# Kernel optimization log

Measured on AMD Instinct MI355X. Metric: run time of the kernel, lower is better.

The kernel has to match this reference:

```python
import jax, jax.numpy as jnp
import numpy as np

U, I, K = 50000, 30000, 64
D0, D1 = 768, 128
N_INTER = 1_000_000
N_LAYERS = 3
BATCH = 4096
EPS = 1e-12


def setup_inputs() -> dict:
    key = jax.random.key(0)
    k1, k2, k3, k4 = jax.random.split(key, 4)
    rng = np.random.default_rng(0)
    # bidirectional bipartite edges: user u <-> item node (U + i)
    u = rng.integers(0, U, size=N_INTER)
    i = rng.integers(0, I, size=N_INTER) + U
    src = np.concatenate([u, i])
    dst = np.concatenate([i, u])
    edge_index = jnp.asarray(np.stack([src, dst]), dtype=jnp.int32)  # [2, 2*N_INTER]
    return {
        "Gu": jax.random.normal(k1, (U, K), dtype=jnp.float32) * 0.1,
        "F0": jax.random.normal(k2, (I, D0), dtype=jnp.float32),
        "F1": jax.random.normal(k3, (I, D1), dtype=jnp.float32),
        "proj_w": jax.random.normal(k4, (D0 + D1, K), dtype=jnp.float32) * 0.03,
        "proj_b": jnp.zeros((K,), dtype=jnp.float32),
        "edge_index": edge_index,
        "user_idx": jnp.asarray(rng.integers(0, U, size=BATCH), dtype=jnp.int32),
        "item_idx": jnp.asarray(rng.integers(0, I, size=BATCH), dtype=jnp.int32),
    }


def _l2_normalize(x):
    # torch.nn.functional.normalize(p=2, dim=1) with eps clamp
    n = jnp.maximum(jnp.linalg.norm(x, axis=1, keepdims=True), EPS)
    return x / n


def reference(Gu, F0, F1, proj_w, proj_b, edge_index, user_idx, item_idx):
    N = U + I
    # concat aggregation: project concatenated multimodal features, L2-normalize rows
    F_proj = _l2_normalize(jnp.concatenate([F0, F1], axis=-1) @ proj_w + proj_b)
    x = jnp.concatenate([Gu, F_proj], axis=0)  # [N, K]

    src, dst = edge_index[0], edge_index[1]
    # gcn_norm without self-loops (LGConv default): D^{-1/2} A D^{-1/2}
    deg = jax.ops.segment_sum(jnp.ones(src.shape[0], dtype=x.dtype), dst, num_segments=N)
    dinv = jnp.where(deg > 0, jax.lax.rsqrt(jnp.maximum(deg, 1.0)), 0.0)
    norm = dinv[src] * dinv[dst]  # [E]

    layers = [x]
    for _ in range(N_LAYERS):
        msg = layers[-1][src] * norm[:, None]  # [E, K]
        layers.append(jax.ops.segment_sum(msg, dst, num_segments=N))

    all_emb = jnp.mean(jnp.stack(layers, axis=0), axis=0)  # layer-wise mean pooling
    gu, fi = all_emb[:U], all_emb[U:]

    # forward(): batched dot product between selected user/item embeddings
    xui = jnp.sum(gu[user_idx] * fi[item_idx], axis=1)  # [BATCH]
    return xui
```

## Files before the change

kernel.cpp:

```cpp
#include <hip/hip_runtime.h>
#include <hip/hip_bf16.h>

#define NU 50000
#define NI 30000
#define NN 80000
#define KDIM 64
#define DD0 768
#define DD1 128
#define DD 896

#define BROWS 128
#define NB (NN / BROWS)
#define CAPB 5120
#define CAP 96
#define REGION_BYTES 24576
#define ENTS_STRIDE (REGION_BYTES / 4)
#define CHUNK_PAIRS 4096

typedef __attribute__((ext_vector_type(8))) short short8v;
typedef __attribute__((ext_vector_type(4))) short short4v;
typedef __attribute__((ext_vector_type(4))) float float4v;
typedef unsigned short ushort_t;

struct bf16pair { short hi, lo; };

__device__ inline bf16pair f32_split_bf16(float v) {
    __hip_bfloat16 h = __float2bfloat16(v);
    float hf = __bfloat162float(h);
    __hip_bfloat16 l = __float2bfloat16(v - hf);
    bf16pair p;
    p.hi = *reinterpret_cast<short*>(&h);
    p.lo = *reinterpret_cast<short*>(&l);
    return p;
}

__device__ inline float bf16bits_to_f32(ushort_t u) {
    return __uint_as_float(((unsigned int)u) << 16);
}

__device__ inline ushort_t f32_to_bf16_rne(float f) {
    unsigned int u = __float_as_uint(f);
    unsigned int r = (u + 0x7FFFu + ((u >> 16) & 1u)) >> 16;
    return (ushort_t)r;
}

__global__ void wtcvt_kernel(const float* __restrict__ W,
                             short* __restrict__ WTh, short* __restrict__ WTl)
{
    const int i = blockIdx.x * 256 + threadIdx.x;
    if (i < DD * KDIM) {
        const int k = i >> 6, col = i & 63;
        const bf16pair p = f32_split_bf16(W[i]);
        WTh[col * DD + k] = p.hi;
        WTl[col * DD + k] = p.lo;
    }
}

__global__ __launch_bounds__(256) void proj_kernel(
    const float* __restrict__ F0, const float* __restrict__ F1,
    const short* __restrict__ WTh, const short* __restrict__ WTl,
    const float* __restrict__ b, const float* __restrict__ dinv,
    float* __restrict__ Fp, ushort_t* __restrict__ curS)
{
    __shared__ short Ah[64][72];
    __shared__ short Al[64][72];
    __shared__ short Bh[64][72];
    __shared__ short Bl[64][72];

    const int tid  = threadIdx.x;
    const int wv   = tid >> 6;
    const int lane = tid & 63;
    const int lr   = lane & 15;
    const int grp  = lane >> 4;
    const int rowBase = blockIdx.x * 64;

    const int aR[4] = { (0*256+tid) >> 4, (1*256+tid) >> 4,
                        (2*256+tid) >> 4, (3*256+tid) >> 4 };
    const int aK    = (tid & 15) * 4;
    const int bCol[2] = { (0*256+tid) >> 3, (1*256+tid) >> 3 };
    const int bK      = (tid & 7) * 8;

    float4   pA[4];
    short8v  pBh[2], pBl[2];

    auto loadChunk = [&](int c) {
        #pragma unroll
        for (int rep = 0; rep < 4; ++rep) {
            const int r = rowBase + aR[rep];
            float4 v = make_float4(0.f, 0.f, 0.f, 0.f);
            if (r < NI) {
                if (c < 12)
                    v = *(const float4*)&F0[(size_t)r * DD0 + c * 64 + aK];
                else
                    v = *(const float4*)&F1[(size_t)r * DD1 + (c - 12) * 64 + aK];
            }
            pA[rep] = v;
        }
        #pragma unroll
        for (int rep = 0; rep < 2; ++rep) {
            pBh[rep] = *(const short8v*)&WTh[(size_t)bCol[rep] * DD + c * 64 + bK];
            pBl[rep] = *(const short8v*)&WTl[(size_t)bCol[rep] * DD + c * 64 + bK];
        }
    };

    float4v acc[4] = {};

    loadChunk(0);
    for (int c = 0; c < 14; ++c) {
        #pragma unroll
        for (int rep = 0; rep < 4; ++rep) {
            const float4 v = pA[rep];
            const bf16pair p0 = f32_split_bf16(v.x);
            const bf16pair p1 = f32_split_bf16(v.y);
            const bf16pair p2 = f32_split_bf16(v.z);
            const bf16pair p3 = f32_split_bf16(v.w);
            short4v h4, l4;
            h4[0] = p0.hi; h4[1] = p1.hi; h4[2] = p2.hi; h4[3] = p3.hi;
            l4[0] = p0.lo; l4[1] = p1.lo; l4[2] = p2.lo; l4[3] = p3.lo;
            *(short4v*)&Ah[aR[rep]][aK] = h4;
            *(short4v*)&Al[aR[rep]][aK] = l4;
        }
        #pragma unroll
        for (int rep = 0; rep < 2; ++rep) {
            *(short8v*)&Bh[bCol[rep]][bK] = pBh[rep];
            *(short8v*)&Bl[bCol[rep]][bK] = pBl[rep];
        }
        if (c < 13) loadChunk(c + 1);
        __syncthreads();

        #pragma unroll
        for (int ks = 0; ks < 2; ++ks) {
            const int ko = ks * 32 + grp * 8;
            const short8v ah = *(const short8v*)&Ah[wv * 16 + lr][ko];
            const short8v al = *(const short8v*)&Al[wv * 16 + lr][ko];
            #pragma unroll
            for (int nt = 0; nt < 4; ++nt) {
                const short8v bh = *(const short8v*)&Bh[nt * 16 + lr][ko];
                const short8v bl = *(const short8v*)&Bl[nt * 16 + lr][ko];
                acc[nt] = __builtin_amdgcn_mfma_f32_16x16x32_bf16(ah, bh, acc[nt], 0, 0, 0);
                acc[nt] = __builtin_amdgcn_mfma_f32_16x16x32_bf16(ah, bl, acc[nt], 0, 0, 0);
                acc[nt] = __builtin_amdgcn_mfma_f32_16x16x32_bf16(al, bh, acc[nt], 0, 0, 0);
            }
        }
        __syncthreads();
    }

    float bias[4];
    #pragma unroll
    for (int nt = 0; nt < 4; ++nt) bias[nt] = b[nt * 16 + lr];

    float y[4][4];
    float ssp[4];
    #pragma unroll
    for (int i = 0; i < 4; ++i) {
        ssp[i] = 0.f;
        #pragma unroll
        for (int nt = 0; nt < 4; ++nt) {
            y[nt][i] = acc[nt][i] + bias[nt];
            ssp[i] += y[nt][i] * y[nt][i];
        }
    }
    #pragma unroll
    for (int i = 0; i < 4; ++i) {
        float ss = ssp[i];
        ss += __shfl_xor(ss, 1);
        ss += __shfl_xor(ss, 2);
        ss += __shfl_xor(ss, 4);
        ss += __shfl_xor(ss, 8);
        const int r = rowBase + wv * 16 + 4 * grp + i;
        if (r < NI) {
            const float inv = 1.0f / fmaxf(sqrtf(ss), 1e-12f);
            const float dv  = dinv[NU + r];
            #pragma unroll
            for (int nt = 0; nt < 4; ++nt) {
                const float o = y[nt][i] * inv;
                Fp[(size_t)(NU + r) * KDIM + nt * 16 + lr] = o;
                curS[(size_t)(NU + r) * KDIM + nt * 16 + lr] = f32_to_bf16_rne(o * dv);
            }
        }
    }
}

__global__ void userinit_kernel(const float* __restrict__ Gu,
                                const float* __restrict__ dinv,
                                ushort_t* __restrict__ curS)
{
    const int i = blockIdx.x * blockDim.x + threadIdx.x;
    if (i < NU * KDIM / 4) {
        const int row = i >> 4;
        const float dv = dinv[row];
        const float4 g = ((const float4*)Gu)[i];
        short4v s;
        s[0] = (short)f32_to_bf16_rne(g.x * dv);
        s[1] = (short)f32_to_bf16_rne(g.y * dv);
        s[2] = (short)f32_to_bf16_rne(g.z * dv);
        s[3] = (short)f32_to_bf16_rne(g.w * dv);
        *(short4v*)&curS[(size_t)i * 4] = s;
    }
}

__global__ __launch_bounds__(256) void part_kernel(
    const int* __restrict__ src, const int* __restrict__ dst,
    int* __restrict__ bcur, unsigned int* __restrict__ ents, int E2)
{
    __shared__ int bcntL[NB];
    __shared__ int bposL[NB];
    const int tid = threadIdx.x;
    const int pairBase = blockIdx.x * CHUNK_PAIRS;

    for (int i = tid; i < NB; i += 256) bcntL[i] = 0;
    __syncthreads();

    #pragma unroll
    for (int it = 0; it < CHUNK_PAIRS / 256; ++it) {
        const int p = pairBase + it * 256 + tid;
        if (p < E2) {
            const int u  = src[p];
            const int iF = dst[p];
            atomicAdd(&bcntL[iF >> 7], 1);
            atomicAdd(&bcntL[u  >> 7], 1);
        }
    }
    __syncthreads();

    for (int bkt = tid; bkt < NB; bkt += 256) {
        const int c = bcntL[bkt];
        bposL[bkt] = (c > 0) ? atomicAdd(&bcur[bkt], c) : 0;
        bcntL[bkt] = 0;
    }
    __syncthreads();

    #pragma unroll
    for (int it = 0; it < CHUNK_PAIRS / 256; ++it) {
        const int p = pairBase + it * 256 + tid;
        if (p < E2) {
            const int u  = src[p];
            const int iF = dst[p];
            {
                const int bkt = iF >> 7;
                const int k = bposL[bkt] + atomicAdd(&bcntL[bkt], 1);
                if (k < CAPB)
                    ents[(size_t)bkt * ENTS_STRIDE + k] =
                        ((unsigned int)(iF & 127) << 16) | (unsigned int)u;
            }
            {
                const int bkt = u >> 7;
                const int k = bposL[bkt] + atomicAdd(&bcntL[bkt], 1);
                if (k < CAPB)
                    ents[(size_t)bkt * ENTS_STRIDE + k] =
                        ((unsigned int)(u & 127) << 16) | (unsigned int)(iF - NU);
            }
        }
    }
}

__global__ __launch_bounds__(256) void toELL_kernel(
    const int* __restrict__ bcur, unsigned int* __restrict__ ents,
    ushort_t* __restrict__ col,
    int* __restrict__ cnt, float* __restrict__ dinv)
{
    __shared__ unsigned int eL[CAPB];
    __shared__ int curL[BROWS];
    const int bkt = blockIdx.x;
    const int tid = threadIdx.x;

    int n = bcur[bkt]; n = (n < CAPB) ? n : CAPB;
    const unsigned int* ep = ents + (size_t)bkt * ENTS_STRIDE;

    for (int j = tid; j < n; j += 256) eL[j] = ep[j];
    if (tid < BROWS) curL[tid] = 0;
    __syncthreads();

    const size_t rowB = (size_t)bkt * BROWS;
    for (int j = tid; j < n; j += 256) {
        const unsigned int e = eL[j];
        const int dl = (int)(e >> 16);
        const int slot = atomicAdd(&curL[dl], 1);
        if (slot < CAP)
            col[(rowB + dl) * CAP + slot] = (ushort_t)(e & 0xFFFFu);
    }
    __syncthreads();

    if (tid < BROWS) {
        int c = curL[tid];
        c = (c < CAP) ? c : CAP;
        const size_t row = rowB + tid;
        cnt[row]  = c;
        dinv[row] = (c > 0) ? rsqrtf((float)c) : 0.0f;
    }
}

__global__ __launch_bounds__(256) void pull_kernel(
    const ushort_t* __restrict__ curS, ushort_t* __restrict__ nxtS,
    const int* __restrict__ cnt,
    const ushort_t* __restrict__ col,
    const float* __restrict__ dinv,
    int rowStart, int nRows)
{
    const int wid = __builtin_amdgcn_readfirstlane(
        (int)((blockIdx.x * blockDim.x + threadIdx.x) >> 6));
    const int lane = threadIdx.x & 63;
    if (wid >= nRows) return;
    const int row = rowStart + wid;

    const unsigned int* cpd = (const unsigned int*)(col + (size_t)row * CAP);
    const int addB = (row < NU) ? NU : 0;
    const int n = cnt[row];

    float a0 = 0.f, a1 = 0.f, a2 = 0.f, a3 = 0.f;
    int j = 0;
    for (; j + 8 <= n; j += 8) {
        const uint4 cc = *(const uint4*)(cpd + (j >> 1));
        const int c0 = (int)(cc.x & 0xFFFFu) + addB;
        const int c1 = (int)(cc.x >> 16)     + addB;
        const int c2 = (int)(cc.y & 0xFFFFu) + addB;
        const int c3 = (int)(cc.y >> 16)     + addB;
        const int c4 = (int)(cc.z & 0xFFFFu) + addB;
        const int c5 = (int)(cc.z >> 16)     + addB;
        const int c6 = (int)(cc.w & 0xFFFFu) + addB;
        const int c7 = (int)(cc.w >> 16)     + addB;
        const float v0 = bf16bits_to_f32(curS[((size_t)c0 << 6) + lane]);
        const float v1 = bf16bits_to_f32(curS[((size_t)c1 << 6) + lane]);
        const float v2 = bf16bits_to_f32(curS[((size_t)c2 << 6) + lane]);
        const float v3 = bf16bits_to_f32(curS[((size_t)c3 << 6) + lane]);
        const float v4 = bf16bits_to_f32(curS[((size_t)c4 << 6) + lane]);
        const float v5 = bf16bits_to_f32(curS[((size_t)c5 << 6) + lane]);
        const float v6 = bf16bits_to_f32(curS[((size_t)c6 << 6) + lane]);
        const float v7 = bf16bits_to_f32(curS[((size_t)c7 << 6) + lane]);
        a0 += v0 + v4; a1 += v1 + v5; a2 += v2 + v6; a3 += v3 + v7;
    }
    for (; j < n; ++j) {
        const unsigned int d = cpd[j >> 1];
        const int c = (int)((j & 1) ? (d >> 16) : (d & 0xFFFFu)) + addB;
        a0 += bf16bits_to_f32(curS[((size_t)c << 6) + lane]);
    }

    const float dv = dinv[row];
    nxtS[((size_t)row << 6) + lane] =
        f32_to_bf16_rne(dv * dv * ((a0 + a1) + (a2 + a3)));
}

__device__ inline float row_acc(int row, float x0, int lane,
                                const ushort_t* __restrict__ S1,
                                const ushort_t* __restrict__ S2,
                                const int* __restrict__ cnt,
                                const ushort_t* __restrict__ col,
                                const float* __restrict__ dinv)
{
    const float dv  = dinv[row];
    const float rdv = (dv > 0.f) ? 1.0f / dv : 0.0f;
    const float s1 = bf16bits_to_f32(S1[((size_t)row << 6) + lane]);
    const float s2 = bf16bits_to_f32(S2[((size_t)row << 6) + lane]);

    const unsigned int* cpd = (const unsigned int*)(col + (size_t)row * CAP);
    const int addB = (row < NU) ? NU : 0;
    const int n = cnt[row];
    float a0 = 0.f, a1 = 0.f, a2 = 0.f, a3 = 0.f;
    int j = 0;
    for (; j + 8 <= n; j += 8) {
        const uint4 cc = *(const uint4*)(cpd + (j >> 1));
        const int c0 = (int)(cc.x & 0xFFFFu) + addB;
        const int c1 = (int)(cc.x >> 16)     + addB;
        const int c2 = (int)(cc.y & 0xFFFFu) + addB;
        const int c3 = (int)(cc.y >> 16)     + addB;
        const int c4 = (int)(cc.z & 0xFFFFu) + addB;
        const int c5 = (int)(cc.z >> 16)     + addB;
        const int c6 = (int)(cc.w & 0xFFFFu) + addB;
        const int c7 = (int)(cc.w >> 16)     + addB;
        const float v0 = bf16bits_to_f32(S2[((size_t)c0 << 6) + lane]);
        const float v1 = bf16bits_to_f32(S2[((size_t)c1 << 6) + lane]);
        const float v2 = bf16bits_to_f32(S2[((size_t)c2 << 6) + lane]);
        const float v3 = bf16bits_to_f32(S2[((size_t)c3 << 6) + lane]);
        const float v4 = bf16bits_to_f32(S2[((size_t)c4 << 6) + lane]);
        const float v5 = bf16bits_to_f32(S2[((size_t)c5 << 6) + lane]);
        const float v6 = bf16bits_to_f32(S2[((size_t)c6 << 6) + lane]);
        const float v7 = bf16bits_to_f32(S2[((size_t)c7 << 6) + lane]);
        a0 += v0 + v4; a1 += v1 + v5; a2 += v2 + v6; a3 += v3 + v7;
    }
    for (; j < n; ++j) {
        const unsigned int d = cpd[j >> 1];
        const int c = (int)((j & 1) ? (d >> 16) : (d & 0xFFFFu)) + addB;
        a0 += bf16bits_to_f32(S2[((size_t)c << 6) + lane]);
    }

    return x0 + (s1 + s2) * rdv + dv * ((a0 + a1) + (a2 + a3));
}

__global__ __launch_bounds__(256) void out_kernel(
    const float* __restrict__ Gu, const float* __restrict__ Fp,
    const ushort_t* __restrict__ S1, const ushort_t* __restrict__ S2,
    const int* __restrict__ cnt, const ushort_t* __restrict__ col,
    const float* __restrict__ dinv,
    const int* __restrict__ uidx, const int* __restrict__ iidx,
    float* __restrict__ out, int B)
{
    const int wid = __builtin_amdgcn_readfirstlane(
        (int)((blockIdx.x * blockDim.x + threadIdx.x) >> 6));
    const int lane = threadIdx.x & 63;
    if (wid >= B) return;
    const int u  = uidx[wid];
    const int rI = NU + iidx[wid];

    const float au = row_acc(u,  Gu[((size_t)u  << 6) + lane], lane,
                             S1, S2, cnt, col, dinv);
    const float ai = row_acc(rI, Fp[((size_t)rI << 6) + lane], lane,
                             S1, S2, cnt, col, dinv);
    float p = au * ai;
    #pragma unroll
    for (int m = 32; m >= 1; m >>= 1) p += __shfl_xor(p, m);
    if (lane == 0) out[wid] = p * (1.0f / 16.0f);
}

extern "C" void kernel_launch(void* const* d_in, const int* in_sizes, int n_in,
                              void* d_out, int out_size, void* d_ws, size_t ws_size,
                              hipStream_t stream)
{
    const float* Gu = (const float*)d_in[0];
    const float* F0 = (const float*)d_in[1];
    const float* F1 = (const float*)d_in[2];
    const float* W  = (const float*)d_in[3];
    const float* pb = (const float*)d_in[4];
    const int* edge = (const int*)d_in[5];
    const int* uidx = (const int*)d_in[6];
    const int* iidx = (const int*)d_in[7];
    const int E  = in_sizes[5] / 2;
    const int E2 = E / 2;
    const int B = in_sizes[6];
    const int* srcp = edge;
    const int* dstp = edge + E;

    const size_t XE = (size_t)NN * KDIM;
    float*    Fp    = (float*)d_ws;
    ushort_t* curA  = (ushort_t*)(Fp + XE);
    ushort_t* curB  = curA + XE;
    float*    dinv  = (float*)(curB + XE);
    int*      cnt   = (int*)(dinv + NN);
    int*      bcur  = cnt + NN;
    short*    WTh   = (short*)(bcur + NB);
    short*    WTl   = WTh + (size_t)KDIM * DD;
    ushort_t* col   = (ushort_t*)(WTl + (size_t)KDIM * DD);
    unsigned int* ents = (unsigned int*)col;

    (void)hipMemsetAsync(bcur, 0, NB * sizeof(int), stream);
    part_kernel<<<(E2 + CHUNK_PAIRS - 1) / CHUNK_PAIRS, 256, 0, stream>>>(
        srcp, dstp, bcur, ents, E2);
    toELL_kernel<<<NB, 256, 0, stream>>>(bcur, ents, col, cnt, dinv);

    wtcvt_kernel<<<(DD * KDIM + 255) / 256, 256, 0, stream>>>(W, WTh, WTl);

    userinit_kernel<<<(NU * KDIM / 4 + 255) / 256, 256, 0, stream>>>(
        Gu, dinv, curA);
    proj_kernel<<<(NI + 63) / 64, 256, 0, stream>>>(F0, F1, WTh, WTl, pb,
                                                    dinv, Fp, curA);

    const int gridU = (NU * 64 + 255) / 256;
    const int gridI = (NI * 64 + 255) / 256;
    pull_kernel<<<gridU, 256, 0, stream>>>(curA, curB, cnt, col, dinv, 0, NU);
    pull_kernel<<<gridI, 256, 0, stream>>>(curA, curB, cnt, col, dinv, NU, NI);
    pull_kernel<<<gridU, 256, 0, stream>>>(curB, curA, cnt, col, dinv, 0, NU);
    pull_kernel<<<gridI, 256, 0, stream>>>(curB, curA, cnt, col, dinv, NU, NI);

    out_kernel<<<(int)(((size_t)B * 64 + 255) / 256), 256, 0, stream>>>(
        Gu, Fp, curB, curA, cnt, col, dinv, uidx, iidx, (float*)d_out, B);
}
```

Measured before the change: 178.3 us.

## Process two rows per wave in pull kernel and double-buffer projection prefetch

The graph pull kernel now assigns a pair of rows to each wave. Each half-wave gathers a full 64-wide bf16 row using 32-bit loads of packed element pairs, which halves the wave count and the number of gather instructions. The projection GEMM prefetches two chunks ahead with ping-pong register buffers to hide global latency better. The pull kernel risks divergence and a slow scalar tail when the two rows in a pair have different degrees, and the prefetch raises register pressure.

```diff
diff --git a/kernel.cpp b/kernel.cpp
--- a/kernel.cpp
+++ b/kernel.cpp
@@ -80,10 +80,11 @@
     const int bCol[2] = { (0*256+tid) >> 3, (1*256+tid) >> 3 };
     const int bK      = (tid & 7) * 8;
 
-    float4   pA[4];
-    short8v  pBh[2], pBl[2];
-
-    auto loadChunk = [&](int c) {
+    float4   pA0[4], pA1[4];
+    short8v  pBh0[2], pBl0[2], pBh1[2], pBl1[2];
+
+    auto loadChunk = [&](int c, float4 (&qA)[4],
+                         short8v (&qBh)[2], short8v (&qBl)[2]) {
         #pragma unroll
         for (int rep = 0; rep < 4; ++rep) {
             const int r = rowBase + aR[rep];
@@ -94,22 +95,22 @@
                 else
                     v = *(const float4*)&F1[(size_t)r * DD1 + (c - 12) * 64 + aK];
             }
-            pA[rep] = v;
+            qA[rep] = v;
         }
         #pragma unroll
         for (int rep = 0; rep < 2; ++rep) {
-            pBh[rep] = *(const short8v*)&WTh[(size_t)bCol[rep] * DD + c * 64 + bK];
-            pBl[rep] = *(const short8v*)&WTl[(size_t)bCol[rep] * DD + c * 64 + bK];
+            qBh[rep] = *(const short8v*)&WTh[(size_t)bCol[rep] * DD + c * 64 + bK];
+            qBl[rep] = *(const short8v*)&WTl[(size_t)bCol[rep] * DD + c * 64 + bK];
         }
     };
 
     float4v acc[4] = {};
 
-    loadChunk(0);
-    for (int c = 0; c < 14; ++c) {
+    auto step = [&](int c, float4 (&qA)[4],
+                    short8v (&qBh)[2], short8v (&qBl)[2]) {
         #pragma unroll
         for (int rep = 0; rep < 4; ++rep) {
-            const float4 v = pA[rep];
+            const float4 v = qA[rep];
             const bf16pair p0 = f32_split_bf16(v.x);
             const bf16pair p1 = f32_split_bf16(v.y);
             const bf16pair p2 = f32_split_bf16(v.z);
@@ -122,10 +123,10 @@
         }
         #pragma unroll
         for (int rep = 0; rep < 2; ++rep) {
-            *(short8v*)&Bh[bCol[rep]][bK] = pBh[rep];
-            *(short8v*)&Bl[bCol[rep]][bK] = pBl[rep];
-        }
-        if (c < 13) loadChunk(c + 1);
+            *(short8v*)&Bh[bCol[rep]][bK] = qBh[rep];
+            *(short8v*)&Bl[bCol[rep]][bK] = qBl[rep];
+        }
+        if (c + 2 < 14) loadChunk(c + 2, qA, qBh, qBl);
         __syncthreads();
 
         #pragma unroll
@@ -143,6 +144,14 @@
             }
         }
         __syncthreads();
+    };
+
+    loadChunk(0, pA0, pBh0, pBl0);
+    loadChunk(1, pA1, pBh1, pBl1);
+    #pragma unroll
+    for (int c = 0; c < 14; c += 2) {
+        step(c,     pA0, pBh0, pBl0);
+        step(c + 1, pA1, pBh1, pBl1);
     }
 
     float bias[4];
@@ -295,49 +304,82 @@
     const int* __restrict__ cnt,
     const ushort_t* __restrict__ col,
     const float* __restrict__ dinv,
-    int rowStart, int nRows)
-{
-    const int wid = __builtin_amdgcn_readfirstlane(
+    int rowStart, int nPairs)
+{
+    const int pr = __builtin_amdgcn_readfirstlane(
         (int)((blockIdx.x * blockDim.x + threadIdx.x) >> 6));
     const int lane = threadIdx.x & 63;
-    if (wid >= nRows) return;
-    const int row = rowStart + wid;
-
-    const unsigned int* cpd = (const unsigned int*)(col + (size_t)row * CAP);
-    const int addB = (row < NU) ? NU : 0;
-    const int n = cnt[row];
-
-    float a0 = 0.f, a1 = 0.f, a2 = 0.f, a3 = 0.f;
+    const int sub  = lane & 31;
+    const int h    = lane >> 5;
+    if (pr >= nPairs) return;
+    const int row0 = rowStart + pr * 2;
+    const int rowH = row0 + h;
+    const int addB = (row0 < NU) ? NU : 0;
+    const int n0 = cnt[row0];
+    const int n1 = cnt[row0 + 1];
+    const int nH   = h ? n1 : n0;
+    const int nMin = (n0 < n1) ? n0 : n1;
+    const int nMax = (n0 < n1) ? n1 : n0;
+    const unsigned int* cp0 = (const unsigned int*)(col + (size_t)row0 * CAP);
+    const unsigned int* cp1 = (const unsigned int*)(col + ((size_t)row0 + 1) * CAP);
+
+    float aLo0 = 0.f, aLo1 = 0.f, aHi0 = 0.f, aHi1 = 0.f;
     int j = 0;
-    for (; j + 8 <= n; j += 8) {
-        const uint4 cc = *(const uint4*)(cpd + (j >> 1));
-        const int c0 = (int)(cc.x & 0xFFFFu) + addB;
-        const int c1 = (int)(cc.x >> 16)     + addB;
-        const int c2 = (int)(cc.y & 0xFFFFu) + addB;
-        const int c3 = (int)(cc.y >> 16)     + addB;
-        const int c4 = (int)(cc.z & 0xFFFFu) + addB;
-        const int c5 = (int)(cc.z >> 16)     + addB;
-        const int c6 = (int)(cc.w & 0xFFFFu) + addB;
-        const int c7 = (int)(cc.w >> 16)     + addB;
-        const float v0 = bf16bits_to_f32(curS[((size_t)c0 << 6) + lane]);
-        const float v1 = bf16bits_to_f32(curS[((size_t)c1 << 6) + lane]);
-        const float v2 = bf16bits_to_f32(curS[((size_t)c2 << 6) + lane]);
-        const float v3 = bf16bits_to_f32(curS[((size_t)c3 << 6) + lane]);
-        const float v4 = bf16bits_to_f32(curS[((size_t)c4 << 6) + lane]);
-        const float v5 = bf16bits_to_f32(curS[((size_t)c5 << 6) + lane]);
-        const float v6 = bf16bits_to_f32(curS[((size_t)c6 << 6) + lane]);
-        const float v7 = bf16bits_to_f32(curS[((size_t)c7 << 6) + lane]);
-        a0 += v0 + v4; a1 += v1 + v5; a2 += v2 + v6; a3 += v3 + v7;
-    }
-    for (; j < n; ++j) {
-        const unsigned int d = cpd[j >> 1];
-        const int c = (int)((j & 1) ? (d >> 16) : (d & 0xFFFFu)) + addB;
-        a0 += bf16bits_to_f32(curS[((size_t)c << 6) + lane]);
-    }
-
-    const float dv = dinv[row];
-    nxtS[((size_t)row << 6) + lane] =
-        f32_to_bf16_rne(dv * dv * ((a0 + a1) + (a2 + a3)));
+    for (; j + 8 <= nMin; j += 8) {
+        const uint4 D0 = *(const uint4*)(cp0 + (j >> 1));
+        const uint4 D1 = *(const uint4*)(cp1 + (j >> 1));
+        const unsigned int dx = h ? D1.x : D0.x;
+        const unsigned int dy = h ? D1.y : D0.y;
+        const unsigned int dz = h ? D1.z : D0.z;
+        const unsigned int dw = h ? D1.w : D0.w;
+        const int c0 = (int)(dx & 0xFFFFu) + addB;
+        const int c1 = (int)(dx >> 16)     + addB;
+        const int c2 = (int)(dy & 0xFFFFu) + addB;
+        const int c3 = (int)(dy >> 16)     + addB;
+        const int c4 = (int)(dz & 0xFFFFu) + addB;
+        const int c5 = (int)(dz >> 16)     + addB;
+        const int c6 = (int)(dw & 0xFFFFu) + addB;
+        const int c7 = (int)(dw >> 16)     + addB;
+        const unsigned int v0 = *(const unsigned int*)&curS[((size_t)c0 << 6) + sub * 2];
+        const unsigned int v1 = *(const unsigned int*)&curS[((size_t)c1 << 6) + sub * 2];
+        const unsigned int v2 = *(const unsigned int*)&curS[((size_t)c2 << 6) + sub * 2];
+        const unsigned int v3 = *(const unsigned int*)&curS[((size_t)c3 << 6) + sub * 2];
+        const unsigned int v4 = *(const unsigned int*)&curS[((size_t)c4 << 6) + sub * 2];
+        const unsigned int v5 = *(const unsigned int*)&curS[((size_t)c5 << 6) + sub * 2];
+        const unsigned int v6 = *(const unsigned int*)&curS[((size_t)c6 << 6) + sub * 2];
+        const unsigned int v7 = *(const unsigned int*)&curS[((size_t)c7 << 6) + sub * 2];
+        aLo0 += __uint_as_float(v0 << 16) + __uint_as_float(v2 << 16);
+        aLo1 += __uint_as_float(v1 << 16) + __uint_as_float(v3 << 16);
+        aHi0 += __uint_as_float(v0 & 0xFFFF0000u) + __uint_as_float(v2 & 0xFFFF0000u);
+        aHi1 += __uint_as_float(v1 & 0xFFFF0000u) + __uint_as_float(v3 & 0xFFFF0000u);
+        aLo0 += __uint_as_float(v4 << 16) + __uint_as_float(v6 << 16);
+        aLo1 += __uint_as_float(v5 << 16) + __uint_as_float(v7 << 16);
+        aHi0 += __uint_as_float(v4 & 0xFFFF0000u) + __uint_as_float(v6 & 0xFFFF0000u);
+        aHi1 += __uint_as_float(v5 & 0xFFFF0000u) + __uint_as_float(v7 & 0xFFFF0000u);
+    }
+    for (; j < nMax; j += 2) {
+        const unsigned int d0 = cp0[j >> 1];
+        const unsigned int d1 = cp1[j >> 1];
+        const unsigned int d  = h ? d1 : d0;
+        if (j < nH) {
+            const int c = (int)(d & 0xFFFFu) + addB;
+            const unsigned int v = *(const unsigned int*)&curS[((size_t)c << 6) + sub * 2];
+            aLo0 += __uint_as_float(v << 16);
+            aHi0 += __uint_as_float(v & 0xFFFF0000u);
+        }
+        if (j + 1 < nH) {
+            const int c = (int)(d >> 16) + addB;
+            const unsigned int v = *(const unsigned int*)&curS[((size_t)c << 6) + sub * 2];
+            aLo1 += __uint_as_float(v << 16);
+            aHi1 += __uint_as_float(v & 0xFFFF0000u);
+        }
+    }
+
+    const float dv = dinv[rowH];
+    const float f = dv * dv;
+    const unsigned int w = (unsigned int)f32_to_bf16_rne((aLo0 + aLo1) * f)
+                         | ((unsigned int)f32_to_bf16_rne((aHi0 + aHi1) * f) << 16);
+    ((unsigned int*)&nxtS[(size_t)rowH << 6])[sub] = w;
 }
 
 __device__ inline float row_acc(int row, float x0, int lane,
@@ -453,12 +495,12 @@
     proj_kernel<<<(NI + 63) / 64, 256, 0, stream>>>(F0, F1, WTh, WTl, pb,
                                                     dinv, Fp, curA);
 
-    const int gridU = (NU * 64 + 255) / 256;
-    const int gridI = (NI * 64 + 255) / 256;
-    pull_kernel<<<gridU, 256, 0, stream>>>(curA, curB, cnt, col, dinv, 0, NU);
-    pull_kernel<<<gridI, 256, 0, stream>>>(curA, curB, cnt, col, dinv, NU, NI);
-    pull_kernel<<<gridU, 256, 0, stream>>>(curB, curA, cnt, col, dinv, 0, NU);
-    pull_kernel<<<gridI, 256, 0, stream>>>(curB, curA, cnt, col, dinv, NU, NI);
+    const int gridU = (NU / 2 * 64 + 255) / 256;
+    const int gridI = (NI / 2 * 64 + 255) / 256;
+    pull_kernel<<<gridU, 256, 0, stream>>>(curA, curB, cnt, col, dinv, 0,  NU / 2);
+    pull_kernel<<<gridI, 256, 0, stream>>>(curA, curB, cnt, col, dinv, NU, NI / 2);
+    pull_kernel<<<gridU, 256, 0, stream>>>(curB, curA, cnt, col, dinv, 0,  NU / 2);
+    pull_kernel<<<gridI, 256, 0, stream>>>(curB, curA, cnt, col, dinv, NU, NI / 2);
 
     out_kernel<<<(int)(((size_t)B * 64 + 255) / 256), 256, 0, stream>>>(
         Gu, Fp, curB, curA, cnt, col, dinv, uidx, iidx, (float*)d_out, B);
```

New measurement: 178.3 us. Within noise of the previous version (+0.0%).
